# Kernel optimization log

Hardware: AMD Instinct MI355X
Metric: run time of the kernel (lower is better)

Reference implementation:

```python
import jax, jax.numpy as jnp
import numpy as np

D_MODEL = 512
NUM_HEADS = 8
DEPTH = D_MODEL // NUM_HEADS


def setup_inputs() -> dict:
    key = jax.random.key(0)
    ks = jax.random.split(key, 9)
    B, S = 2, 2048
    x = jax.random.normal(ks[0], (B, S, D_MODEL), dtype=jnp.float32)
    s = 1.0 / np.sqrt(D_MODEL)
    Wq = jax.random.uniform(ks[1], (D_MODEL, D_MODEL), minval=-s, maxval=s)
    bq = jax.random.uniform(ks[2], (D_MODEL,), minval=-s, maxval=s)
    Wk = jax.random.uniform(ks[3], (D_MODEL, D_MODEL), minval=-s, maxval=s)
    bk = jax.random.uniform(ks[4], (D_MODEL,), minval=-s, maxval=s)
    Wv = jax.random.uniform(ks[5], (D_MODEL, D_MODEL), minval=-s, maxval=s)
    bv = jax.random.uniform(ks[6], (D_MODEL,), minval=-s, maxval=s)
    Wo = jax.random.uniform(ks[7], (D_MODEL, D_MODEL), minval=-s, maxval=s)
    bo = jax.random.uniform(ks[8], (D_MODEL,), minval=-s, maxval=s)
    return {"x": x, "Wq": Wq, "bq": bq, "Wk": Wk, "bk": bk,
            "Wv": Wv, "bv": bv, "Wo": Wo, "bo": bo}


def _split_heads(t, B, S):
    # [B,S,D] -> [B,H,S,depth]
    return t.reshape(B, S, NUM_HEADS, DEPTH).transpose(0, 2, 1, 3)


def reference(x, Wq, bq, Wk, bk, Wv, bv, Wo, bo):
    B, S, _ = x.shape
    q = _split_heads(x @ Wq.T + bq, B, S) / jnp.sqrt(jnp.float32(DEPTH))
    k = _split_heads(x @ Wk.T + bk, B, S)
    v = _split_heads(x @ Wv.T + bv, B, S)
    scores = jnp.einsum('bhsd,bhtd->bhst', q, k)  # [B,H,S,S]
    attn = jax.nn.softmax(scores, axis=-1)
    out = jnp.einsum('bhst,bhtd->bhsd', attn, v)  # [B,H,S,depth]
    out = out.transpose(0, 2, 1, 3).reshape(B, S, D_MODEL)
    return out @ Wo.T + bo
```

## Files before the change

### kernel.cpp

```cpp
#include <hip/hip_runtime.h>

typedef unsigned int   uint32;
typedef unsigned short ushort16;

constexpr int BATCH = 2;
constexpr int SEQ   = 2048;
constexpr int DM    = 512;
constexpr int NH    = 8;
constexpr int DP    = 64;
constexpr int MROWS = BATCH * SEQ;
constexpr size_t HEADS_ELEMS = (size_t)BATCH * NH * SEQ * DP;

typedef short bf16x8 __attribute__((ext_vector_type(8)));
typedef float f32x4  __attribute__((ext_vector_type(4)));
typedef float f32x16 __attribute__((ext_vector_type(16)));
#define MFMA16(a, b, c) __builtin_amdgcn_mfma_f32_16x16x32_bf16((a), (b), (c), 0, 0, 0)
#define MFMA32(a, b, c) __builtin_amdgcn_mfma_f32_32x32x16_bf16((a), (b), (c), 0, 0, 0)

__device__ __forceinline__ ushort16 f2bf(float f) {
    uint32 u = __float_as_uint(f);
    uint32 r = (u + 0x7fffu + ((u >> 16) & 1u)) >> 16;
    return (ushort16)r;
}

__device__ __forceinline__ uint32 cvtpk(float a, float b) {
    uint32 r;
    asm("v_cvt_pk_bf16_f32 %0, %1, %2" : "=v"(r) : "v"(a), "v"(b));
    return r;
}

__device__ __forceinline__ bf16x8 mkfrag(uint32 u0, uint32 u1, uint32 u2, uint32 u3) {
    union { uint32 u[4]; bf16x8 v; } t;
    t.u[0] = u0; t.u[1] = u1; t.u[2] = u2; t.u[3] = u3;
    return t.v;
}

__device__ __forceinline__ void gload16(const void* g, void* l) {
    __builtin_amdgcn_global_load_lds(
        (const __attribute__((address_space(1))) unsigned int*)g,
        (__attribute__((address_space(3))) unsigned int*)l, 16, 0, 0);
}

constexpr int XF4 = (MROWS * DM) / 4;
constexpr int WF4 = (DM * DM) / 4;

__global__ __launch_bounds__(256)
void convert_inputs(const float4* __restrict__ x,  const float4* __restrict__ wq,
                    const float4* __restrict__ wk, const float4* __restrict__ wv,
                    const float4* __restrict__ wo, ushort4* __restrict__ xb,
                    ushort4* __restrict__ wqkv, ushort4* __restrict__ wob) {
    const int idx = blockIdx.x * 256 + threadIdx.x;
    float4 v; ushort4* dp;
    if (idx < XF4) { v = x[idx]; dp = xb + idx; }
    else {
        const int r = idx - XF4;
        if (r < WF4)          { v = wq[r];           dp = wqkv + r; }
        else if (r < 2 * WF4) { v = wk[r - WF4];     dp = wqkv + r; }
        else if (r < 3 * WF4) { v = wv[r - 2 * WF4]; dp = wqkv + r; }
        else                  { v = wo[r - 3 * WF4]; dp = wob + (r - 3 * WF4); }
    }
    ushort4 o = {f2bf(v.x), f2bf(v.y), f2bf(v.z), f2bf(v.w)};
    *dp = o;
}

template <int BM, int BN, int EPI>
__global__ __launch_bounds__(256)
void gemm_mfma(const ushort16* __restrict__ X, const ushort16* __restrict__ Wc,
               const float* __restrict__ bq_, const float* __restrict__ bk_,
               const float* __restrict__ bv_, const float* __restrict__ bo_,
               ushort16* __restrict__ Qh, ushort16* __restrict__ Kh,
               ushort16* __restrict__ Vt, float* __restrict__ Out,
               float qscale) {
    constexpr int FM = BM / 32;
    constexpr int FN = BN / 32;
    __shared__ ushort16 As[BM * 64];
    __shared__ ushort16 Bs[BN * 64];

    const int tid  = threadIdx.x;
    const int lane = tid & 63;
    const int wid  = tid >> 6;
    const int lg   = lane >> 4;
    const int lq   = lane & 15;
    const int wr   = wid >> 1;
    const int wc   = wid & 1;
    const int m0   = blockIdx.y * BM;
    const int n0   = blockIdx.x * BN;
    const bool swapped = (EPI == 1) || (n0 < 2 * DM);

    f32x4 acc[FM][FN];
    #pragma unroll
    for (int i = 0; i < FM; i++)
        #pragma unroll
        for (int j = 0; j < FN; j++)
            #pragma unroll
            for (int r = 0; r < 4; r++) acc[i][j][r] = 0.f;

    for (int k0 = 0; k0 < DM; k0 += 64) {
        #pragma unroll
        for (int i = 0; i < BM / 32; i++) {
            const int ch = tid + i * 256;
            const int row = ch >> 3, c8 = (ch & 7) * 8;
            gload16(X + (size_t)(m0 + row) * DM + k0 + c8, As + (size_t)ch * 8);
        }
        #pragma unroll
        for (int i = 0; i < BN / 32; i++) {
            const int ch = tid + i * 256;
            const int row = ch >> 3, c8 = (ch & 7) * 8;
            gload16(Wc + (size_t)(n0 + row) * DM + k0 + c8, Bs + (size_t)ch * 8);
        }
        __syncthreads();

        bf16x8 af[FM][2], bfr[FN][2];
        #pragma unroll
        for (int i = 0; i < FM; i++)
            #pragma unroll
            for (int kk = 0; kk < 2; kk++)
                af[i][kk] = *(const bf16x8*)(As + (size_t)(wr * (BM / 2) + i * 16 + lq) * 64 + kk * 32 + lg * 8);
        #pragma unroll
        for (int j = 0; j < FN; j++)
            #pragma unroll
            for (int kk = 0; kk < 2; kk++)
                bfr[j][kk] = *(const bf16x8*)(Bs + (size_t)(wc * (BN / 2) + j * 16 + lq) * 64 + kk * 32 + lg * 8);

        if (swapped) {
            #pragma unroll
            for (int kk = 0; kk < 2; kk++)
                #pragma unroll
                for (int i = 0; i < FM; i++)
                    #pragma unroll
                    for (int j = 0; j < FN; j++)
                        acc[i][j] = MFMA16(bfr[j][kk], af[i][kk], acc[i][j]);
        } else {
            #pragma unroll
            for (int kk = 0; kk < 2; kk++)
                #pragma unroll
                for (int i = 0; i < FM; i++)
                    #pragma unroll
                    for (int j = 0; j < FN; j++)
                        acc[i][j] = MFMA16(af[i][kk], bfr[j][kk], acc[i][j]);
        }
        __syncthreads();
    }

    if (EPI == 1) {
        #pragma unroll
        for (int i = 0; i < FM; i++) {
            const int m = m0 + wr * (BM / 2) + i * 16 + lq;
            #pragma unroll
            for (int j = 0; j < FN; j++) {
                const int nr = n0 + wc * (BN / 2) + j * 16 + lg * 4;
                float4 b4 = *(const float4*)(bo_ + nr);
                float4 o;
                o.x = acc[i][j][0] + b4.x; o.y = acc[i][j][1] + b4.y;
                o.z = acc[i][j][2] + b4.z; o.w = acc[i][j][3] + b4.w;
                *(float4*)(Out + (size_t)m * DM + nr) = o;
            }
        }
    } else if (n0 < 2 * DM) {
        #pragma unroll
        for (int i = 0; i < FM; i++) {
            const int m = m0 + wr * (BM / 2) + i * 16 + lq;
            const int b = m >> 11, s = m & (SEQ - 1);
            #pragma unroll
            for (int j = 0; j < FN; j++) {
                const int nr = n0 + wc * (BN / 2) + j * 16 + lg * 4;
                const bool isq = nr < DM;
                const int rel = nr & (DM - 1);
                const int h = rel >> 6, d = rel & 63;
                float4 b4 = *(const float4*)((isq ? bq_ : bk_) + rel);
                const float sc = isq ? qscale : 1.0f;
                ushort4 o = { f2bf((acc[i][j][0] + b4.x) * sc),
                              f2bf((acc[i][j][1] + b4.y) * sc),
                              f2bf((acc[i][j][2] + b4.z) * sc),
                              f2bf((acc[i][j][3] + b4.w) * sc) };
                ushort16* dst = (isq ? Qh : Kh) +
                    (((size_t)(b * NH + h) * SEQ + s) * DP + d);
                *(ushort4*)dst = o;
            }
        }
    } else {
        #pragma unroll
        for (int j = 0; j < FN; j++) {
            const int n = n0 + wc * (BN / 2) + j * 16 + lq;
            const int rel = n - 2 * DM;
            const int h = rel >> 6, d = rel & 63;
            const float bias = bv_[rel];
            #pragma unroll
            for (int i = 0; i < FM; i++) {
                const int mr = m0 + wr * (BM / 2) + i * 16 + lg * 4;
                const int b = mr >> 11, s0 = mr & (SEQ - 1);
                ushort4 o = { f2bf(acc[i][j][0] + bias),
                              f2bf(acc[i][j][1] + bias),
                              f2bf(acc[i][j][2] + bias),
                              f2bf(acc[i][j][3] + bias) };
                ushort16* dst = Vt +
                    (((size_t)(b * NH + h) * DP + d) * SEQ + s0);
                *(ushort4*)dst = o;
            }
        }
    }
}

__global__ __launch_bounds__(1024, 1)
void attn_mfma(const ushort16* __restrict__ Q, const ushort16* __restrict__ K,
               const ushort16* __restrict__ Vt, ushort16* __restrict__ O) {
    __shared__ ushort16 Kl[3][128 * 64];
    __shared__ ushort16 Vl[3][64 * 128];
    __shared__ float    lbuf[4][4][32];

    const int tid  = threadIdx.x;
    const int lane = tid & 63;
    const int wid  = tid >> 6;
    const int qw   = wid & 3;
    const int kw   = wid >> 2;
    const int h    = lane >> 5;
    const int l31  = lane & 31;
    const int l7   = l31 & 7;

    const int bid = blockIdx.x;
    const int w   = (bid & 7) * 32 + (bid >> 3);
    const int qt  = w & 15;
    const int bh  = w >> 4;

    const int qrow = qt * 128 + qw * 32 + l31;
    const ushort16* qbase = Q + ((size_t)bh * SEQ + qrow) * DP;
    bf16x8 qf[4];
    #pragma unroll
    for (int ds = 0; ds < 4; ds++)
        qf[ds] = *(const bf16x8*)(qbase + ds * 16 + h * 8);

    f32x16 ok0, ok1;
    #pragma unroll
    for (int r = 0; r < 16; r++) { ok0[r] = 0.f; ok1[r] = 0.f; }
    float lrun = 0.f;

    const ushort16* kg = K  + (size_t)bh * SEQ * DP;
    const ushort16* vg = Vt + (size_t)bh * DP * SEQ;
    const int kr = tid >> 3, kc = tid & 7;
    const int ksrc = (kc ^ (kr & 7)) * 8;
    const ushort16* const kgp = kg + (size_t)kr * DP + ksrc;
    const int vr = tid >> 4, vc = tid & 15;
    const int vsrc = (vc ^ (vr & 7)) * 8;
    const ushort16* const vgp = vg + (size_t)vr * SEQ + vsrc;

    auto stage = [&](int buf, int t) {
        gload16(kgp + (size_t)t * 128 * DP, &Kl[buf][(size_t)tid * 8]);
        gload16(vgp + (size_t)t * 128,      &Vl[buf][(size_t)tid * 8]);
    };

    const int krow = kw * 32 + l31;
    int koff[4];
    #pragma unroll
    for (int ds = 0; ds < 4; ds++)
        koff[ds] = krow * 64 + (((ds * 2 + h) ^ l7) * 8);
    int voff[2][2];
    #pragma unroll
    for (int dt = 0; dt < 2; dt++)
        #pragma unroll
        for (int kc2 = 0; kc2 < 2; kc2++)
            voff[dt][kc2] = (dt * 32 + l31) * 128 + (((kw * 4 + kc2 * 2 + h) ^ l7) * 8);

    auto compute = [&](int buf) {
        const ushort16* kb = &Kl[buf][0];
        const ushort16* vb = &Vl[buf][0];
        f32x16 st;
        #pragma unroll
        for (int r = 0; r < 16; r++) st[r] = 0.f;
        __builtin_amdgcn_s_setprio(1);
        #pragma unroll
        for (int ds = 0; ds < 4; ds++) {
            bf16x8 kf = *(const bf16x8*)(kb + koff[ds]);
            st = MFMA32(kf, qf[ds], st);
        }
        __builtin_amdgcn_s_setprio(0);

        #pragma unroll
        for (int r = 0; r < 16; r++) {
            st[r] = __builtin_exp2f(st[r]);
            lrun += st[r];
        }

        uint32 A0 = cvtpk(st[0], st[1]),   A1 = cvtpk(st[2], st[3]);
        uint32 B0 = cvtpk(st[4], st[5]),   B1 = cvtpk(st[6], st[7]);
        uint32 C0 = cvtpk(st[8], st[9]),   C1 = cvtpk(st[10], st[11]);
        uint32 D0 = cvtpk(st[12], st[13]), D1 = cvtpk(st[14], st[15]);
        uint32 z0 = __shfl_xor((int)(h ? A0 : B0), 32);
        uint32 z1 = __shfl_xor((int)(h ? A1 : B1), 32);
        uint32 z2 = __shfl_xor((int)(h ? C0 : D0), 32);
        uint32 z3 = __shfl_xor((int)(h ? C1 : D1), 32);
        bf16x8 pa0 = h ? mkfrag(z0, z1, B0, B1) : mkfrag(A0, A1, z0, z1);
        bf16x8 pa1 = h ? mkfrag(z2, z3, D0, D1) : mkfrag(C0, C1, z2, z3);

        const bf16x8 v00 = *(const bf16x8*)(vb + voff[0][0]);
        const bf16x8 v01 = *(const bf16x8*)(vb + voff[0][1]);
        const bf16x8 v10 = *(const bf16x8*)(vb + voff[1][0]);
        const bf16x8 v11 = *(const bf16x8*)(vb + voff[1][1]);
        __builtin_amdgcn_s_setprio(1);
        ok0 = MFMA32(pa0, v00, ok0);
        ok0 = MFMA32(pa1, v01, ok0);
        ok1 = MFMA32(pa0, v10, ok1);
        ok1 = MFMA32(pa1, v11, ok1);
        __builtin_amdgcn_s_setprio(0);
    };

    #define WAITN(n) asm volatile("s_waitcnt vmcnt(" #n ")" ::: "memory")
    #define BAR() __builtin_amdgcn_s_barrier()

    stage(0, 0);
    stage(1, 1);
    int t = 0;
    #pragma unroll 1
    for (int it = 0; it < 4; ++it) {
        WAITN(2); BAR(); stage(2, t + 2); compute(0);
        WAITN(2); BAR(); stage(0, t + 3); compute(1);
        WAITN(2); BAR(); stage(1, t + 4); compute(2);
        t += 3;
    }
    WAITN(2); BAR(); stage(2, 14); compute(0);
    WAITN(2); BAR(); stage(0, 15); compute(1);
    WAITN(2); BAR(); compute(2);
    WAITN(0); BAR(); compute(0);
    #undef WAITN
    #undef BAR

    lrun += __shfl_xor(lrun, 32);

    __syncthreads();
    float* const fK = (float*)&Kl[0][0];
    float* const fV = (float*)&Vl[0][0];
    if (h == 0) lbuf[qw][kw][l31] = lrun;
    if (kw > 0) {
        const int ridx = (kw - 1) * 4 + qw;
        float* const dst = (ridx < 6) ? (fK + ridx * 2048) : (fV + (ridx - 6) * 2048);
        #pragma unroll
        for (int r = 0; r < 16; r++) {
            const int q = (r & 3) + 8 * (r >> 2) + 4 * h;
            dst[q * 64 + l31]      = ok0[r];
            dst[q * 64 + 32 + l31] = ok1[r];
        }
    }
    __syncthreads();
    if (kw == 0) {
        float* const p1 = fK + qw * 2048;
        float* const p2 = (qw < 2) ? (fK + (4 + qw) * 2048)
                                   : (fV + (qw - 2) * 2048);
        float* const p3 = fV + (2 + qw) * 2048;
        const float lsum = lbuf[qw][0][l31] + lbuf[qw][1][l31]
                         + lbuf[qw][2][l31] + lbuf[qw][3][l31];
        const float linv = 1.f / lsum;
        const int b = bh >> 3, hh = bh & 7;
        #pragma unroll
        for (int r = 0; r < 16; r++) {
            const int q = (r & 3) + 8 * (r >> 2) + 4 * h;
            const float li_q = __shfl(linv, q);
            const int o0 = q * 64 + l31;
            const int o1 = q * 64 + 32 + l31;
            const float v0 = (ok0[r] + p1[o0] + p2[o0] + p3[o0]) * li_q;
            const float v1 = (ok1[r] + p1[o1] + p2[o1] + p3[o1]) * li_q;
            const int qr = qt * 128 + qw * 32 + q;
            ushort16* orow = O + ((size_t)(b * SEQ + qr)) * DM + hh * DP;
            orow[l31]      = f2bf(v0);
            orow[32 + l31] = f2bf(v1);
        }
    }
}

extern "C" void kernel_launch(void* const* d_in, const int* in_sizes, int n_in,
                              void* d_out, int out_size, void* d_ws, size_t ws_size,
                              hipStream_t stream) {
    const float* x  = (const float*)d_in[0];
    const float* Wq = (const float*)d_in[1];
    const float* bq = (const float*)d_in[2];
    const float* Wk = (const float*)d_in[3];
    const float* bk = (const float*)d_in[4];
    const float* Wv = (const float*)d_in[5];
    const float* bv = (const float*)d_in[6];
    const float* Wo = (const float*)d_in[7];
    const float* bo = (const float*)d_in[8];
    float* out = (float*)d_out;

    ushort16* ws   = (ushort16*)d_ws;
    ushort16* xb   = ws;
    ushort16* wqkv = xb + (size_t)MROWS * DM;
    ushort16* wob  = wqkv + (size_t)3 * DM * DM;
    ushort16* qh   = wob + (size_t)DM * DM;
    ushort16* kh   = qh + HEADS_ELEMS;
    ushort16* vt   = kh + HEADS_ELEMS;
    ushort16* oh   = vt + HEADS_ELEMS;

    convert_inputs<<<dim3((XF4 + 4 * WF4) / 256), dim3(256), 0, stream>>>(
        (const float4*)x, (const float4*)Wq, (const float4*)Wk,
        (const float4*)Wv, (const float4*)Wo,
        (ushort4*)xb, (ushort4*)wqkv, (ushort4*)wob);

    const float qscale = 0.125f * 1.44269504088896f;

    gemm_mfma<128, 64, 0><<<dim3(24, 32), dim3(256), 0, stream>>>(
        xb, wqkv, bq, bk, bv, bo, qh, kh, vt, nullptr, qscale);

    attn_mfma<<<dim3(256), dim3(1024), 0, stream>>>(qh, kh, vt, oh);

    gemm_mfma<64, 64, 1><<<dim3(8, 64), dim3(256), 0, stream>>>(
        oh, wob, bq, bk, bv, bo, qh, kh, vt, out, qscale);
}
```

Measured before the change: 65.97 us.

## Split attention over key halves across blocks with separate merge kernel

The attention kernel is restructured from 256 blocks of 1024 threads into 512 blocks of 512 threads, where each block handles half of the key sequence and each wave processes two 32-row key groups per tile. Staging moves from triple to double buffering. Unnormalized partial outputs and row sums go to fp32 workspace, and a new merge kernel adds the halves, normalizes and writes bf16. The aim is more blocks per CU and better occupancy and latency hiding, at the cost of an extra launch and extra global traffic for the fp32 partials.

Result: slower. 70.57 us (+7.0%).

```diff
diff --git a/kernel.cpp b/kernel.cpp
--- a/kernel.cpp
+++ b/kernel.cpp
@@ -201,12 +201,13 @@
     }
 }
 
-__global__ __launch_bounds__(1024, 1)
+__global__ __launch_bounds__(512, 4)
 void attn_mfma(const ushort16* __restrict__ Q, const ushort16* __restrict__ K,
-               const ushort16* __restrict__ Vt, ushort16* __restrict__ O) {
-    __shared__ ushort16 Kl[3][128 * 64];
-    __shared__ ushort16 Vl[3][64 * 128];
-    __shared__ float    lbuf[4][4][32];
+               const ushort16* __restrict__ Vt, float* __restrict__ pO,
+               float* __restrict__ pL) {
+    __shared__ ushort16 Kl[2][128 * 64];
+    __shared__ ushort16 Vl[2][64 * 128];
+    __shared__ float    lbuf[4][2][32];
 
     const int tid  = threadIdx.x;
     const int lane = tid & 63;
@@ -218,9 +219,10 @@
     const int l7   = l31 & 7;
 
     const int bid = blockIdx.x;
-    const int w   = (bid & 7) * 32 + (bid >> 3);
-    const int qt  = w & 15;
-    const int bh  = w >> 4;
+    const int w   = (bid & 7) * 64 + (bid >> 3);
+    const int kh2 = w & 1;
+    const int qt  = (w >> 1) & 15;
+    const int bh  = w >> 5;
 
     const int qrow = qt * 128 + qw * 32 + l31;
     const ushort16* qbase = Q + ((size_t)bh * SEQ + qrow) * DP;
@@ -234,92 +236,102 @@
     for (int r = 0; r < 16; r++) { ok0[r] = 0.f; ok1[r] = 0.f; }
     float lrun = 0.f;
 
-    const ushort16* kg = K  + (size_t)bh * SEQ * DP;
-    const ushort16* vg = Vt + (size_t)bh * DP * SEQ;
-    const int kr = tid >> 3, kc = tid & 7;
-    const int ksrc = (kc ^ (kr & 7)) * 8;
-    const ushort16* const kgp = kg + (size_t)kr * DP + ksrc;
-    const int vr = tid >> 4, vc = tid & 15;
-    const int vsrc = (vc ^ (vr & 7)) * 8;
-    const ushort16* const vgp = vg + (size_t)vr * SEQ + vsrc;
+    const int kbase = kh2 * 1024;
+    const ushort16* kg = K  + ((size_t)bh * SEQ + kbase) * DP;
+    const ushort16* vg = Vt + (size_t)bh * DP * SEQ + kbase;
+    const int kr0 = tid >> 3, kc0 = tid & 7;
+    const ushort16* const kgp0 = kg + (size_t)kr0 * DP + ((kc0 ^ (kr0 & 7)) * 8);
+    const ushort16* const kgp1 = kg + (size_t)(kr0 + 64) * DP + ((kc0 ^ ((kr0 + 64) & 7)) * 8);
+    const int vr0 = tid >> 4, vc0 = tid & 15;
+    const ushort16* const vgp0 = vg + (size_t)vr0 * SEQ + ((vc0 ^ (vr0 & 7)) * 8);
+    const ushort16* const vgp1 = vg + (size_t)(vr0 + 32) * SEQ + ((vc0 ^ ((vr0 + 32) & 7)) * 8);
 
     auto stage = [&](int buf, int t) {
-        gload16(kgp + (size_t)t * 128 * DP, &Kl[buf][(size_t)tid * 8]);
-        gload16(vgp + (size_t)t * 128,      &Vl[buf][(size_t)tid * 8]);
+        const size_t ko = (size_t)t * 128 * DP;
+        const size_t vo = (size_t)t * 128;
+        gload16(kgp0 + ko, &Kl[buf][(size_t)tid * 8]);
+        gload16(kgp1 + ko, &Kl[buf][(size_t)(tid + 512) * 8]);
+        gload16(vgp0 + vo, &Vl[buf][(size_t)tid * 8]);
+        gload16(vgp1 + vo, &Vl[buf][(size_t)(tid + 512) * 8]);
     };
 
-    const int krow = kw * 32 + l31;
-    int koff[4];
+    int koff[2][4];
     #pragma unroll
-    for (int ds = 0; ds < 4; ds++)
-        koff[ds] = krow * 64 + (((ds * 2 + h) ^ l7) * 8);
-    int voff[2][2];
+    for (int rg = 0; rg < 2; rg++) {
+        const int krow = kw * 64 + rg * 32 + l31;
+        #pragma unroll
+        for (int ds = 0; ds < 4; ds++)
+            koff[rg][ds] = krow * 64 + (((ds * 2 + h) ^ l7) * 8);
+    }
+    int voff[2][2][2];
     #pragma unroll
     for (int dt = 0; dt < 2; dt++)
         #pragma unroll
-        for (int kc2 = 0; kc2 < 2; kc2++)
-            voff[dt][kc2] = (dt * 32 + l31) * 128 + (((kw * 4 + kc2 * 2 + h) ^ l7) * 8);
+        for (int rg = 0; rg < 2; rg++)
+            #pragma unroll
+            for (int kc = 0; kc < 2; kc++)
+                voff[dt][rg][kc] = (dt * 32 + l31) * 128 +
+                    (((kw * 8 + rg * 4 + kc * 2 + h) ^ l7) * 8);
 
     auto compute = [&](int buf) {
         const ushort16* kb = &Kl[buf][0];
         const ushort16* vb = &Vl[buf][0];
-        f32x16 st;
-        #pragma unroll
-        for (int r = 0; r < 16; r++) st[r] = 0.f;
-        __builtin_amdgcn_s_setprio(1);
-        #pragma unroll
-        for (int ds = 0; ds < 4; ds++) {
-            bf16x8 kf = *(const bf16x8*)(kb + koff[ds]);
-            st = MFMA32(kf, qf[ds], st);
-        }
-        __builtin_amdgcn_s_setprio(0);
-
-        #pragma unroll
-        for (int r = 0; r < 16; r++) {
-            st[r] = __builtin_exp2f(st[r]);
-            lrun += st[r];
-        }
-
-        uint32 A0 = cvtpk(st[0], st[1]),   A1 = cvtpk(st[2], st[3]);
-        uint32 B0 = cvtpk(st[4], st[5]),   B1 = cvtpk(st[6], st[7]);
-        uint32 C0 = cvtpk(st[8], st[9]),   C1 = cvtpk(st[10], st[11]);
-        uint32 D0 = cvtpk(st[12], st[13]), D1 = cvtpk(st[14], st[15]);
-        uint32 z0 = __shfl_xor((int)(h ? A0 : B0), 32);
-        uint32 z1 = __shfl_xor((int)(h ? A1 : B1), 32);
-        uint32 z2 = __shfl_xor((int)(h ? C0 : D0), 32);
-        uint32 z3 = __shfl_xor((int)(h ? C1 : D1), 32);
-        bf16x8 pa0 = h ? mkfrag(z0, z1, B0, B1) : mkfrag(A0, A1, z0, z1);
-        bf16x8 pa1 = h ? mkfrag(z2, z3, D0, D1) : mkfrag(C0, C1, z2, z3);
-
-        const bf16x8 v00 = *(const bf16x8*)(vb + voff[0][0]);
-        const bf16x8 v01 = *(const bf16x8*)(vb + voff[0][1]);
-        const bf16x8 v10 = *(const bf16x8*)(vb + voff[1][0]);
-        const bf16x8 v11 = *(const bf16x8*)(vb + voff[1][1]);
-        __builtin_amdgcn_s_setprio(1);
-        ok0 = MFMA32(pa0, v00, ok0);
-        ok0 = MFMA32(pa1, v01, ok0);
-        ok1 = MFMA32(pa0, v10, ok1);
-        ok1 = MFMA32(pa1, v11, ok1);
-        __builtin_amdgcn_s_setprio(0);
+        #pragma unroll
+        for (int rg = 0; rg < 2; rg++) {
+            f32x16 st;
+            #pragma unroll
+            for (int r = 0; r < 16; r++) st[r] = 0.f;
+            __builtin_amdgcn_s_setprio(1);
+            #pragma unroll
+            for (int ds = 0; ds < 4; ds++) {
+                bf16x8 kf = *(const bf16x8*)(kb + koff[rg][ds]);
+                st = MFMA32(kf, qf[ds], st);
+            }
+            __builtin_amdgcn_s_setprio(0);
+
+            #pragma unroll
+            for (int r = 0; r < 16; r++) {
+                st[r] = __builtin_exp2f(st[r]);
+                lrun += st[r];
+            }
+
+            uint32 A0 = cvtpk(st[0], st[1]),   A1 = cvtpk(st[2], st[3]);
+            uint32 B0 = cvtpk(st[4], st[5]),   B1 = cvtpk(st[6], st[7]);
+            uint32 C0 = cvtpk(st[8], st[9]),   C1 = cvtpk(st[10], st[11]);
+            uint32 D0 = cvtpk(st[12], st[13]), D1 = cvtpk(st[14], st[15]);
+            uint32 z0 = __shfl_xor((int)(h ? A0 : B0), 32);
+            uint32 z1 = __shfl_xor((int)(h ? A1 : B1), 32);
+            uint32 z2 = __shfl_xor((int)(h ? C0 : D0), 32);
+            uint32 z3 = __shfl_xor((int)(h ? C1 : D1), 32);
+            bf16x8 pa0 = h ? mkfrag(z0, z1, B0, B1) : mkfrag(A0, A1, z0, z1);
+            bf16x8 pa1 = h ? mkfrag(z2, z3, D0, D1) : mkfrag(C0, C1, z2, z3);
+
+            const bf16x8 v00 = *(const bf16x8*)(vb + voff[0][rg][0]);
+            const bf16x8 v01 = *(const bf16x8*)(vb + voff[0][rg][1]);
+            const bf16x8 v10 = *(const bf16x8*)(vb + voff[1][rg][0]);
+            const bf16x8 v11 = *(const bf16x8*)(vb + voff[1][rg][1]);
+            __builtin_amdgcn_s_setprio(1);
+            ok0 = MFMA32(pa0, v00, ok0);
+            ok0 = MFMA32(pa1, v01, ok0);
+            ok1 = MFMA32(pa0, v10, ok1);
+            ok1 = MFMA32(pa1, v11, ok1);
+            __builtin_amdgcn_s_setprio(0);
+        }
     };
 
     #define WAITN(n) asm volatile("s_waitcnt vmcnt(" #n ")" ::: "memory")
     #define BAR() __builtin_amdgcn_s_barrier()
 
     stage(0, 0);
-    stage(1, 1);
-    int t = 0;
     #pragma unroll 1
-    for (int it = 0; it < 4; ++it) {
-        WAITN(2); BAR(); stage(2, t + 2); compute(0);
-        WAITN(2); BAR(); stage(0, t + 3); compute(1);
-        WAITN(2); BAR(); stage(1, t + 4); compute(2);
-        t += 3;
-    }
-    WAITN(2); BAR(); stage(2, 14); compute(0);
-    WAITN(2); BAR(); stage(0, 15); compute(1);
-    WAITN(2); BAR(); compute(2);
-    WAITN(0); BAR(); compute(0);
+    for (int t = 0; t < 7; ++t) {
+        stage((t + 1) & 1, t + 1);
+        WAITN(4); BAR();
+        compute(t & 1);
+        BAR();
+    }
+    WAITN(0); BAR();
+    compute(1);
     #undef WAITN
     #undef BAR
 
@@ -327,11 +339,9 @@
 
     __syncthreads();
     float* const fK = (float*)&Kl[0][0];
-    float* const fV = (float*)&Vl[0][0];
     if (h == 0) lbuf[qw][kw][l31] = lrun;
-    if (kw > 0) {
-        const int ridx = (kw - 1) * 4 + qw;
-        float* const dst = (ridx < 6) ? (fK + ridx * 2048) : (fV + (ridx - 6) * 2048);
+    if (kw == 1) {
+        float* const dst = fK + qw * 2048;
         #pragma unroll
         for (int r = 0; r < 16; r++) {
             const int q = (r & 3) + 8 * (r >> 2) + 4 * h;
@@ -341,28 +351,48 @@
     }
     __syncthreads();
     if (kw == 0) {
-        float* const p1 = fK + qw * 2048;
-        float* const p2 = (qw < 2) ? (fK + (4 + qw) * 2048)
-                                   : (fV + (qw - 2) * 2048);
-        float* const p3 = fV + (2 + qw) * 2048;
-        const float lsum = lbuf[qw][0][l31] + lbuf[qw][1][l31]
-                         + lbuf[qw][2][l31] + lbuf[qw][3][l31];
-        const float linv = 1.f / lsum;
-        const int b = bh >> 3, hh = bh & 7;
+        const float* const pb = fK + qw * 2048;
+        const int pidx = (bh * 16 + qt) * 2 + kh2;
+        float* const po = pO + (size_t)pidx * 8192;
+        const float lsum = lbuf[qw][0][l31] + lbuf[qw][1][l31];
+        if (h == 0) pL[pidx * 128 + qw * 32 + l31] = lsum;
         #pragma unroll
         for (int r = 0; r < 16; r++) {
             const int q = (r & 3) + 8 * (r >> 2) + 4 * h;
-            const float li_q = __shfl(linv, q);
-            const int o0 = q * 64 + l31;
-            const int o1 = q * 64 + 32 + l31;
-            const float v0 = (ok0[r] + p1[o0] + p2[o0] + p3[o0]) * li_q;
-            const float v1 = (ok1[r] + p1[o1] + p2[o1] + p3[o1]) * li_q;
-            const int qr = qt * 128 + qw * 32 + q;
-            ushort16* orow = O + ((size_t)(b * SEQ + qr)) * DM + hh * DP;
-            orow[l31]      = f2bf(v0);
-            orow[32 + l31] = f2bf(v1);
-        }
-    }
+            po[(qw * 32 + q) * 64 + l31]      = ok0[r] + pb[q * 64 + l31];
+            po[(qw * 32 + q) * 64 + 32 + l31] = ok1[r] + pb[q * 64 + 32 + l31];
+        }
+    }
+}
+
+__global__ __launch_bounds__(256)
+void attn_merge(const float* __restrict__ pO, const float* __restrict__ pL,
+                ushort16* __restrict__ O) {
+    const int u  = blockIdx.x * 256 + threadIdx.x;
+    const int d0 = (u & 7) * 8;
+    const int q  = (u >> 3) & 127;
+    const int qt = (u >> 10) & 15;
+    const int bh = u >> 14;
+
+    const size_t base0 = ((size_t)(bh * 16 + qt) * 2) * 8192 + q * 64 + d0;
+    const size_t base1 = base0 + 8192;
+    const int    li    = (bh * 16 + qt) * 2 * 128 + q;
+
+    const float4 a0 = *(const float4*)(pO + base0);
+    const float4 a1 = *(const float4*)(pO + base0 + 4);
+    const float4 b0 = *(const float4*)(pO + base1);
+    const float4 b1 = *(const float4*)(pO + base1 + 4);
+    const float  inv = 1.f / (pL[li] + pL[li + 128]);
+
+    union { ushort16 s[8]; uint4 v; } o;
+    o.s[0] = f2bf((a0.x + b0.x) * inv); o.s[1] = f2bf((a0.y + b0.y) * inv);
+    o.s[2] = f2bf((a0.z + b0.z) * inv); o.s[3] = f2bf((a0.w + b0.w) * inv);
+    o.s[4] = f2bf((a1.x + b1.x) * inv); o.s[5] = f2bf((a1.y + b1.y) * inv);
+    o.s[6] = f2bf((a1.z + b1.z) * inv); o.s[7] = f2bf((a1.w + b1.w) * inv);
+
+    const int b = bh >> 3, hh = bh & 7;
+    const int s = qt * 128 + q;
+    *(uint4*)(O + ((size_t)(b * SEQ + s)) * DM + hh * DP + d0) = o.v;
 }
 
 extern "C" void kernel_launch(void* const* d_in, const int* in_sizes, int n_in,
@@ -387,6 +417,8 @@
     ushort16* kh   = qh + HEADS_ELEMS;
     ushort16* vt   = kh + HEADS_ELEMS;
     ushort16* oh   = vt + HEADS_ELEMS;
+    float*    pO   = (float*)(oh + HEADS_ELEMS);
+    float*    pL   = pO + (size_t)512 * 8192;
 
     convert_inputs<<<dim3((XF4 + 4 * WF4) / 256), dim3(256), 0, stream>>>(
         (const float4*)x, (const float4*)Wq, (const float4*)Wk,
@@ -398,7 +430,8 @@
     gemm_mfma<128, 64, 0><<<dim3(24, 32), dim3(256), 0, stream>>>(
         xb, wqkv, bq, bk, bv, bo, qh, kh, vt, nullptr, qscale);
 
-    attn_mfma<<<dim3(256), dim3(1024), 0, stream>>>(qh, kh, vt, oh);
+    attn_mfma<<<dim3(512), dim3(512), 0, stream>>>(qh, kh, vt, pO, pL);
+    attn_merge<<<dim3(1024), dim3(256), 0, stream>>>(pO, pL, oh);
 
     gemm_mfma<64, 64, 1><<<dim3(8, 64), dim3(256), 0, stream>>>(
         oh, wob, bq, bk, bv, bo, qh, kh, vt, out, qscale);
```
